# Performance work log

Hardware: AMD Instinct MI355X
Metric: run time of the kernel (lower is better)

Reference implementation:

```python
import jax, jax.numpy as jnp
import numpy as np

BS, IMG, P, GRID, NPATCH = 4, 224, 14, 16, 256
D, HID, NC, NDIST = 384, 2688, 1000, 7
BETA = 0.07
LN_EPS = 1e-6


def setup_inputs() -> dict:
    key = jax.random.key(0)
    ks = jax.random.split(key, 10)
    feat_target = jax.random.normal(ks[0], (BS, NPATCH, D), jnp.float32)
    feat_ref = jax.random.normal(ks[1], (BS, NPATCH, D), jnp.float32)
    labels_ref = jax.random.randint(ks[2], (BS, 1, IMG, IMG), 0, NC, jnp.int32)
    # distractor permutations of the batch (one per distractor sample)
    perms = jnp.argsort(jax.random.uniform(ks[3], (NDIST, BS)), axis=-1).astype(jnp.int32)
    # projector Mlp (fc1 -> GELU -> fc2), xavier-ish scaling
    fc1_w = jax.random.normal(ks[4], (D, HID), jnp.float32) * (1.0 / np.sqrt(D))
    fc1_b = jnp.zeros((HID,), jnp.float32)
    fc2_w = jax.random.normal(ks[5], (HID, D), jnp.float32) * (1.0 / np.sqrt(HID))
    fc2_b = jnp.zeros((D,), jnp.float32)
    ln_w = jnp.ones((D,), jnp.float32)
    ln_b = jnp.zeros((D,), jnp.float32)
    return {"feat_target": feat_target, "feat_ref": feat_ref, "labels_ref": labels_ref,
            "perms": perms, "fc1_w": fc1_w, "fc1_b": fc1_b, "fc2_w": fc2_w,
            "fc2_b": fc2_b, "ln_w": ln_w, "ln_b": ln_b}


def _layer_norm(x, w, b):
    mu = x.mean(-1, keepdims=True)
    var = jnp.mean((x - mu) ** 2, axis=-1, keepdims=True)
    return (x - mu) * jax.lax.rsqrt(var + LN_EPS) * w + b


def _l2norm(x, eps=1e-12):
    n = jnp.sqrt(jnp.sum(x * x, axis=-1, keepdims=True))
    return x / jnp.maximum(n, eps)


def reference(feat_target, feat_ref, labels_ref, perms, fc1_w, fc1_b, fc2_w, fc2_b, ln_w, ln_b):
    bs = feat_target.shape[0]

    def proj_norm(x):
        h = jax.nn.gelu(x @ fc1_w + fc1_b, approximate=False)  # torch nn.GELU (erf)
        return _layer_norm(h @ fc2_w + fc2_b, ln_w, ln_b)

    ft = proj_norm(feat_target)   # (bs, 256, 384)
    fr = proj_norm(feat_ref)      # (bs, 256, 384)

    # patchify ground truth: (bs,1,224,224) -> (bs, 256, 14*14)
    g = labels_ref.reshape(bs, 1, GRID, P, GRID, P).transpose(0, 2, 4, 1, 3, 5)
    g = g.reshape(bs, NPATCH, P * P)
    # per-patch class histogram / (P*P) == one_hot(...).mean(dim=3), without huge one-hot
    seg = (jnp.arange(NPATCH, dtype=jnp.int32)[None, :, None] * NC + g).reshape(bs, -1)
    counts = jax.vmap(lambda s: jax.ops.segment_sum(
        jnp.ones(s.shape, jnp.float32), s, num_segments=NPATCH * NC))(seg)
    label = counts.reshape(bs, NPATCH, NC) / float(P * P)  # (bs, 256, 1000)

    # distractors: block 0 is identity, blocks 1..NDIST are batch permutations
    all_perm = jnp.concatenate([jnp.arange(bs, dtype=perms.dtype)[None], perms], 0)  # (8, bs)
    lab_d = label[all_perm].transpose(1, 0, 2, 3).reshape(bs, -1, NC)   # (bs, 2048, 1000)
    feat_d = fr[all_perm].transpose(1, 0, 2, 3).reshape(bs, -1, D)      # (bs, 2048, 384)

    # cosine-similarity softmax cross attention (soft kNN over labels)
    q = _l2norm(ft)
    k = _l2norm(feat_d)
    attn = jax.nn.softmax(jnp.einsum('bqd,bkd->bqk', q, k) / BETA, axis=-1)
    label_hat = jnp.einsum('bqk,bkc->bqc', attn, lab_d)                 # (bs, 256, 1000)

    label_hat = label_hat.reshape(bs, GRID, GRID, NC).transpose(0, 3, 1, 2)
    # nearest upsample 16x16 -> 224x224 (scale 14 exactly)
    out = jnp.repeat(jnp.repeat(label_hat, P, axis=2), P, axis=3)
    return out
```

## Files before the change

### kernel.cpp

```cpp
#include <hip/hip_runtime.h>

#define BSZ 4
#define NPATCH 256
#define DIM 384
#define HID 2688
#define NCLS 1000
#define KTOT 2048
#define IMGSZ 224
#define PCH 14
#define GRD 16

static constexpr float INV_BETA = 1.0f / 0.07f;
static constexpr float LN_EPS_F = 1e-6f;

typedef unsigned short u16;
typedef unsigned int   u32;
typedef __attribute__((ext_vector_type(8))) __bf16 bf16x8;
typedef __attribute__((ext_vector_type(4))) float  f32x4;

#define WAITVM(n) asm volatile("s_waitcnt vmcnt(" #n ")" ::: "memory")

__device__ __forceinline__ u16 f2bf(float f) {
    u32 u = __float_as_uint(f);
    return (u16)((u + 0x7FFFu + ((u >> 16) & 1u)) >> 16);
}
__device__ __forceinline__ float bf2f(u16 h) {
    return __uint_as_float(((u32)h) << 16);
}
__device__ __forceinline__ f32x4 mfma16(bf16x8 a, bf16x8 b, f32x4 c) {
    return __builtin_amdgcn_mfma_f32_16x16x32_bf16(a, b, c, 0, 0, 0);
}
__device__ __forceinline__ void gll16(const u16* g, u16* l) {
    __builtin_amdgcn_global_load_lds(
        (const __attribute__((address_space(1))) void*)g,
        (__attribute__((address_space(3))) void*)l, 16, 0, 0);
}
__device__ __forceinline__ bf16x8 ld8(const u16* p) {
    return *(const bf16x8*)p;
}
__device__ __forceinline__ int swz(int row, int cseg) {
    return cseg ^ ((row >> 1) & 3);
}

__device__ __forceinline__ void transpose_split_body(
    const float* __restrict__ In, int R, int C, int bx, int by,
    u16* __restrict__ OutHi, u16* __restrict__ OutLo, float (*tile)[33])
{
    int cx = bx * 32, ry = by * 32;
    int t = threadIdx.x;
    int tr = t >> 5, tc = t & 31;
    #pragma unroll
    for (int i = 0; i < 4; ++i)
        tile[tr + i * 8][tc] = In[(size_t)(ry + tr + i * 8) * C + cx + tc];
    __syncthreads();
    int a = t >> 3, seg = t & 7;
    u16 h4[4], l4[4];
    #pragma unroll
    for (int i = 0; i < 4; ++i) {
        float v = tile[seg * 4 + i][a];
        h4[i] = f2bf(v);
        l4[i] = f2bf(v - bf2f(h4[i]));
    }
    size_t off = (size_t)(cx + a) * R + ry + seg * 4;
    *(uint2*)(OutHi + off) = make_uint2((u32)h4[0] | ((u32)h4[1] << 16),
                                        (u32)h4[2] | ((u32)h4[3] << 16));
    *(uint2*)(OutLo + off) = make_uint2((u32)l4[0] | ((u32)l4[1] << 16),
                                        (u32)l4[2] | ((u32)l4[3] << 16));
}

__global__ __launch_bounds__(256) void prep_kernel(
    const float* __restrict__ Xt, const float* __restrict__ Xr,
    const float* __restrict__ fc1w, const float* __restrict__ fc2w,
    const int* __restrict__ labels,
    u16* __restrict__ Xhi, u16* __restrict__ Xlo,
    u16* __restrict__ W1Th, u16* __restrict__ W1Tl,
    u16* __restrict__ W2Th, u16* __restrict__ W2Tl,
    u16* __restrict__ LabT)
{
    __shared__ float tile[32][33];
    __shared__ int hist16[16][NCLS];
    int blk = blockIdx.x, t = threadIdx.x;
    if (blk < 768) {
        int e = (blk * 256 + t) * 4;
        const float* src = (e < 1024 * DIM) ? (Xt + e) : (Xr + e - 1024 * DIM);
        float4 v = *(const float4*)src;
        float x[4] = {v.x, v.y, v.z, v.w};
        u16 h[4], l[4];
        #pragma unroll
        for (int i = 0; i < 4; ++i) {
            h[i] = f2bf(x[i]);
            l[i] = f2bf(x[i] - bf2f(h[i]));
        }
        *(uint2*)(Xhi + e) = make_uint2((u32)h[0] | ((u32)h[1] << 16), (u32)h[2] | ((u32)h[3] << 16));
        *(uint2*)(Xlo + e) = make_uint2((u32)l[0] | ((u32)l[1] << 16), (u32)l[2] | ((u32)l[3] << 16));
    } else if (blk < 1776) {
        int i = blk - 768;
        transpose_split_body(fc1w, DIM, HID, i % (HID / 32), i / (HID / 32), W1Th, W1Tl, tile);
    } else if (blk < 2784) {
        int i = blk - 1776;
        transpose_split_body(fc2w, HID, DIM, i % (DIM / 32), i / (DIM / 32), W2Th, W2Tl, tile);
    } else {
        int bp = blk - 2784;
        int b = bp >> 4, py = bp & 15;
        for (int u = t; u < 16 * NCLS; u += 256) ((int*)hist16)[u] = 0;
        __syncthreads();
        const int* lrow = labels + (size_t)b * IMGSZ * IMGSZ + py * PCH * IMGSZ;
        for (int i = t; i < PCH * IMGSZ; i += 256) {
            int lab = lrow[i];
            int px = (i % IMGSZ) / PCH;
            atomicAdd(&hist16[px][lab], 1);
        }
        __syncthreads();
        const float inv = 1.0f / (PCH * PCH);
        for (int u = t; u < 16 * NCLS; u += 256) {
            int c = u >> 4, px = u & 15;
            LabT[((size_t)(b << 10) + c) * 256 + py * 16 + px] =
                f2bf(hist16[px][c] * inv);
        }
    }
}

template<int MODE>
__global__ __launch_bounds__(256) void gemm64(
    const u16* __restrict__ Ahi, const u16* __restrict__ Alo,
    const u16* __restrict__ Bhi, const u16* __restrict__ Blo,
    const float* __restrict__ bias,
    u16* __restrict__ OutHi, u16* __restrict__ OutLo, float* __restrict__ OutF)
{
    constexpr int K  = (MODE == 1) ? HID : DIM;
    constexpr int KS = (MODE == 1) ? HID / 4 : K;
    constexpr int NT = KS / 32;
    constexpr int N  = (MODE == 0) ? HID : DIM;

    __shared__ u16 As_h[3][128 * 32];
    __shared__ u16 As_l[3][128 * 32];
    __shared__ u16 Bs_h[3][64 * 32];
    __shared__ u16 Bs_l[3][64 * 32];

    const int tid = threadIdx.x, lane = tid & 63, wid = tid >> 6;
    const int wm = wid >> 1, wn = wid & 1;
    int n0, m0;
    if constexpr (MODE == 0) {
        int s = (blockIdx.x & 7) * 84 + (blockIdx.x >> 3);
        n0 = (s % 42) * 64;
        m0 = (s / 42) * 128;
    } else {
        n0 = blockIdx.x * 64;
        m0 = blockIdx.y * 128;
    }

    const u16 *a_h, *a_l, *b_h, *b_l;
    if constexpr (MODE == 0) {
        a_h = Ahi + (size_t)m0 * K;   a_l = Alo + (size_t)m0 * K;
        b_h = Bhi + (size_t)n0 * K;   b_l = Blo + (size_t)n0 * K;
    } else {
        const int kbase = blockIdx.z * KS;
        a_h = Ahi + (size_t)m0 * K + kbase;   a_l = Alo + (size_t)m0 * K + kbase;
        b_h = Bhi + (size_t)n0 * K + kbase;   b_l = Blo + (size_t)n0 * K + kbase;
    }

    auto stage = [&](int buf, int k0) {
        #pragma unroll
        for (int j = 0; j < 2; ++j) {
            int g = j * 256 + tid;
            int row = g >> 2, cs = g & 3;
            int col = swz(row, cs) << 3;
            gll16(a_h + (size_t)row * K + k0 + col, &As_h[buf][g * 8]);
            gll16(a_l + (size_t)row * K + k0 + col, &As_l[buf][g * 8]);
        }
        {
            int row = tid >> 2, cs = tid & 3;
            int col = swz(row, cs) << 3;
            gll16(b_h + (size_t)row * K + k0 + col, &Bs_h[buf][tid * 8]);
            gll16(b_l + (size_t)row * K + k0 + col, &Bs_l[buf][tid * 8]);
        }
    };

    const int l15 = lane & 15, cq = lane >> 4;
    int aoff[4], boff[2];
    #pragma unroll
    for (int i = 0; i < 4; ++i) {
        int ra = wm * 64 + i * 16 + l15;
        aoff[i] = ra * 32 + swz(ra, cq) * 8;
    }
    #pragma unroll
    for (int j = 0; j < 2; ++j) {
        int rb = wn * 32 + j * 16 + l15;
        boff[j] = rb * 32 + swz(rb, cq) * 8;
    }

    f32x4 acc[4][2] = {};

    auto compute = [&](int buf) {
        bf16x8 ah[4], al[4], bh[2], bl[2];
        #pragma unroll
        for (int i = 0; i < 4; ++i) {
            ah[i] = ld8(&As_h[buf][aoff[i]]);
            al[i] = ld8(&As_l[buf][aoff[i]]);
        }
        #pragma unroll
        for (int j = 0; j < 2; ++j) {
            bh[j] = ld8(&Bs_h[buf][boff[j]]);
            bl[j] = ld8(&Bs_l[buf][boff[j]]);
        }
        #pragma unroll
        for (int mi = 0; mi < 4; ++mi)
            #pragma unroll
            for (int ni = 0; ni < 2; ++ni) {
                acc[mi][ni] = mfma16(ah[mi], bh[ni], acc[mi][ni]);
                acc[mi][ni] = mfma16(ah[mi], bl[ni], acc[mi][ni]);
                acc[mi][ni] = mfma16(al[mi], bh[ni], acc[mi][ni]);
            }
    };

    stage(0, 0);
    stage(1, 32);
    int cur = 0;
    for (int t = 0; t < NT - 1; ++t) {
        WAITVM(6);
        __builtin_amdgcn_s_barrier();
        __builtin_amdgcn_sched_barrier(0);
        if (t + 2 < NT) {
            int nb = cur + 2; if (nb >= 3) nb -= 3;
            stage(nb, (t + 2) * 32);
        }
        compute(cur);
        cur = (cur == 2) ? 0 : cur + 1;
    }
    WAITVM(0);
    __builtin_amdgcn_s_barrier();
    __builtin_amdgcn_sched_barrier(0);
    compute(cur);

    #pragma unroll
    for (int mi = 0; mi < 4; ++mi)
        #pragma unroll
        for (int ni = 0; ni < 2; ++ni)
            #pragma unroll
            for (int r = 0; r < 4; ++r) {
                int gm = m0 + wm * 64 + mi * 16 + cq * 4 + r;
                int gn = n0 + wn * 32 + ni * 16 + l15;
                float v = acc[mi][ni][r];
                if constexpr (MODE == 0) {
                    v += bias[gn];
                    v = 0.5f * v * (1.0f + erff(v * 0.7071067811865476f));
                    u16 h = f2bf(v);
                    OutHi[(size_t)gm * N + gn] = h;
                    OutLo[(size_t)gm * N + gn] = f2bf(v - bf2f(h));
                } else {
                    OutF[(size_t)blockIdx.z * (2048 * DIM) + (size_t)gm * N + gn] = v;
                }
            }
}

__global__ __launch_bounds__(256) void qk64(
    const u16* __restrict__ Z, const int* __restrict__ perms,
    u16* __restrict__ E, float* __restrict__ R)
{
    constexpr int NT = DIM / 32;
    __shared__ u16 As[3][64 * 32];
    __shared__ u16 Bs[3][64 * 32];

    const int tid = threadIdx.x, lane = tid & 63, wid = tid >> 6;
    const int wm = wid >> 1, wn = wid & 1;
    const int n0 = blockIdx.x * 64, m0 = blockIdx.y * 64, b = blockIdx.z;
    const int d = n0 >> 8;
    const int apd = (d == 0) ? b : perms[(d - 1) * BSZ + b];

    const u16* a_g = Z + (size_t)(b * NPATCH + m0) * DIM;
    const u16* b_g = Z + (size_t)(1024 + apd * NPATCH + (n0 & 255)) * DIM;

    auto stage = [&](int buf, int k0) {
        int row = tid >> 2, cs = tid & 3;
        int col = swz(row, cs) << 3;
        gll16(a_g + (size_t)row * DIM + k0 + col, &As[buf][tid * 8]);
        gll16(b_g + (size_t)row * DIM + k0 + col, &Bs[buf][tid * 8]);
    };

    const int l15 = lane & 15, cq = lane >> 4;
    int aoff[2], boff[2];
    #pragma unroll
    for (int i = 0; i < 2; ++i) {
        int ra = wm * 32 + i * 16 + l15;
        aoff[i] = ra * 32 + swz(ra, cq) * 8;
        int rb = wn * 32 + i * 16 + l15;
        boff[i] = rb * 32 + swz(rb, cq) * 8;
    }

    f32x4 acc[2][2] = {};
    auto compute = [&](int buf) {
        bf16x8 a[2], bb[2];
        #pragma unroll
        for (int i = 0; i < 2; ++i) {
            a[i] = ld8(&As[buf][aoff[i]]);
            bb[i] = ld8(&Bs[buf][boff[i]]);
        }
        #pragma unroll
        for (int mi = 0; mi < 2; ++mi)
            #pragma unroll
            for (int ni = 0; ni < 2; ++ni)
                acc[mi][ni] = mfma16(a[mi], bb[ni], acc[mi][ni]);
    };

    stage(0, 0);
    stage(1, 32);
    int cur = 0;
    for (int t = 0; t < NT - 1; ++t) {
        WAITVM(2);
        __builtin_amdgcn_s_barrier();
        __builtin_amdgcn_sched_barrier(0);
        if (t + 2 < NT) {
            int nb = cur + 2; if (nb >= 3) nb -= 3;
            stage(nb, (t + 2) * 32);
        }
        compute(cur);
        cur = (cur == 2) ? 0 : cur + 1;
    }
    WAITVM(0);
    __builtin_amdgcn_s_barrier();
    __builtin_amdgcn_sched_barrier(0);
    compute(cur);

    float rp[2][4] = {};
    #pragma unroll
    for (int mi = 0; mi < 2; ++mi)
        #pragma unroll
        for (int ni = 0; ni < 2; ++ni)
            #pragma unroll
            for (int r = 0; r < 4; ++r) {
                int gm = m0 + wm * 32 + mi * 16 + cq * 4 + r;
                int gn = n0 + wn * 32 + ni * 16 + l15;
                float e = expf((acc[mi][ni][r] - 1.0f) * INV_BETA);
                u16 h = f2bf(e);
                E[((size_t)b * NPATCH + gm) * KTOT + gn] = h;
                rp[mi][r] += bf2f(h);
            }
    #pragma unroll
    for (int mi = 0; mi < 2; ++mi)
        #pragma unroll
        for (int r = 0; r < 4; ++r) {
            float v = rp[mi][r];
            #pragma unroll
            for (int off = 1; off < 16; off <<= 1) v += __shfl_xor(v, off);
            if (l15 == 0) {
                int gm = m0 + wm * 32 + mi * 16 + cq * 4 + r;
                atomicAdd(&R[(size_t)b * NPATCH + gm], v);
            }
        }
}

__global__ __launch_bounds__(256) void pv64(
    const u16* __restrict__ E, const u16* __restrict__ LabT,
    const int* __restrict__ perms, float* __restrict__ Lp)
{
    constexpr int KSP = KTOT / 4;
    constexpr int NT  = KSP / 32;
    __shared__ u16 As[3][128 * 32];
    __shared__ u16 Bs[3][64 * 32];

    const int tid = threadIdx.x, lane = tid & 63, wid = tid >> 6;
    const int wm = wid >> 1, wn = wid & 1;
    const int n0 = blockIdx.x * 64, m0 = blockIdx.y * 128;
    const int b = blockIdx.z & 3, ks = blockIdx.z >> 2;
    const int s0 = ks * 2;
    const int apd0 = (s0 == 0) ? b : perms[(s0 - 1) * BSZ + b];
    const int apd1 = perms[s0 * BSZ + b];

    const u16* abase = E + (size_t)(b * NPATCH + m0) * KTOT + ks * KSP;

    auto stage = [&](int buf, int k0) {
        #pragma unroll
        for (int j = 0; j < 2; ++j) {
            int g = j * 256 + tid;
            int row = g >> 2, cs = g & 3;
            int col = swz(row, cs) << 3;
            gll16(abase + (size_t)row * KTOT + k0 + col, &As[buf][g * 8]);
        }
        {
            int apd = (k0 & 256) ? apd1 : apd0;
            int p0 = k0 & 255;
            int row = tid >> 2, cs = tid & 3;
            int col = swz(row, cs) << 3;
            gll16(LabT + ((size_t)(apd << 10) + n0 + row) * 256 + p0 + col,
                  &Bs[buf][tid * 8]);
        }
    };

    const int l15 = lane & 15, cq = lane >> 4;
    int aoff[4], boff[2];
    #pragma unroll
    for (int i = 0; i < 4; ++i) {
        int ra = wm * 64 + i * 16 + l15;
        aoff[i] = ra * 32 + swz(ra, cq) * 8;
    }
    #pragma unroll
    for (int j = 0; j < 2; ++j) {
        int rb = wn * 32 + j * 16 + l15;
        boff[j] = rb * 32 + swz(rb, cq) * 8;
    }

    f32x4 acc[4][2] = {};
    auto compute = [&](int buf) {
        bf16x8 a[4], bb[2];
        #pragma unroll
        for (int i = 0; i < 4; ++i) a[i] = ld8(&As[buf][aoff[i]]);
        #pragma unroll
        for (int j = 0; j < 2; ++j) bb[j] = ld8(&Bs[buf][boff[j]]);
        #pragma unroll
        for (int mi = 0; mi < 4; ++mi)
            #pragma unroll
            for (int ni = 0; ni < 2; ++ni)
                acc[mi][ni] = mfma16(a[mi], bb[ni], acc[mi][ni]);
    };

    stage(0, 0);
    stage(1, 32);
    int cur = 0;
    for (int t = 0; t < NT - 1; ++t) {
        WAITVM(3);
        __builtin_amdgcn_s_barrier();
        __builtin_amdgcn_sched_barrier(0);
        if (t + 2 < NT) {
            int nb = cur + 2; if (nb >= 3) nb -= 3;
            stage(nb, (t + 2) * 32);
        }
        compute(cur);
        cur = (cur == 2) ? 0 : cur + 1;
    }
    WAITVM(0);
    __builtin_amdgcn_s_barrier();
    __builtin_amdgcn_sched_barrier(0);
    compute(cur);

    #pragma unroll
    for (int mi = 0; mi < 4; ++mi)
        #pragma unroll
        for (int ni = 0; ni < 2; ++ni) {
            int gn = n0 + wn * 32 + ni * 16 + l15;
            if (gn < NCLS) {
                #pragma unroll
                for (int r = 0; r < 4; ++r) {
                    int gm = m0 + wm * 64 + mi * 16 + cq * 4 + r;
                    Lp[(((size_t)ks * BSZ + b) * NPATCH + gm) * NCLS + gn] =
                        acc[mi][ni][r];
                }
            }
        }
}

__device__ __forceinline__ float wave_sum(float v) {
    #pragma unroll
    for (int off = 32; off > 0; off >>= 1) v += __shfl_xor(v, off);
    return v;
}

__global__ __launch_bounds__(256) void ln_l2_kernel(
    const float* __restrict__ P0, const float* __restrict__ fc2b,
    const float* __restrict__ w, const float* __restrict__ b,
    u16* __restrict__ Zbf)
{
    const float* P1 = P0 + 1 * 2048 * DIM;
    const float* P2 = P0 + 2 * 2048 * DIM;
    const float* P3 = P0 + 3 * 2048 * DIM;
    int wid = threadIdx.x >> 6, lane = threadIdx.x & 63;
    int row = blockIdx.x * 4 + wid;
    size_t base = (size_t)row * DIM;
    float x[6];
    float s = 0.0f;
    #pragma unroll
    for (int i = 0; i < 6; ++i) {
        int c = lane + 64 * i;
        x[i] = ((P0[base + c] + P1[base + c]) + (P2[base + c] + P3[base + c])) + fc2b[c];
        s += x[i];
    }
    s = wave_sum(s);
    float mu = s * (1.0f / DIM);
    float vs = 0.0f;
    #pragma unroll
    for (int i = 0; i < 6; ++i) { float d = x[i] - mu; vs += d * d; }
    vs = wave_sum(vs);
    float rstd = 1.0f / sqrtf(vs * (1.0f / DIM) + LN_EPS_F);
    float z[6];
    float n2 = 0.0f;
    #pragma unroll
    for (int i = 0; i < 6; ++i) {
        z[i] = (x[i] - mu) * rstd * w[lane + 64 * i] + b[lane + 64 * i];
        n2 += z[i] * z[i];
    }
    n2 = wave_sum(n2);
    float inv = 1.0f / fmaxf(sqrtf(n2), 1e-12f);
    #pragma unroll
    for (int i = 0; i < 6; ++i)
        Zbf[base + lane + 64 * i] = f2bf(z[i] * inv);
}

__global__ __launch_bounds__(256) void upsample_kernel(
    const float* __restrict__ Lp, const float* __restrict__ R,
    float* __restrict__ out)
{
    constexpr size_t S = (size_t)BSZ * NPATCH * NCLS;
    int blk = blockIdx.x;
    int gy = blk & 15;
    int bc = blk >> 4;
    int c = bc % NCLS;
    int b = bc / NCLS;
    __shared__ float vals[GRD];
    int t = threadIdx.x;
    if (t < GRD) {
        int q = b * NPATCH + gy * GRD + t;
        size_t i = (size_t)q * NCLS + c;
        vals[t] = ((Lp[i] + Lp[i + S]) + (Lp[i + 2 * S] + Lp[i + 3 * S])) / R[q];
    }
    __syncthreads();
    float* obase = out + ((size_t)(b * NCLS + c) * IMGSZ + gy * PCH) * IMGSZ;
    for (int idx = t; idx < PCH * 56; idx += 256) {
        int x4 = idx % 56, dy = idx / 56;
        int x0 = x4 * 4;
        f32x4 v = {vals[x0 / PCH], vals[(x0 + 1) / PCH],
                   vals[(x0 + 2) / PCH], vals[(x0 + 3) / PCH]};
        __builtin_nontemporal_store(v, (f32x4*)(obase + dy * IMGSZ + x0));
    }
}

extern "C" void kernel_launch(void* const* d_in, const int* in_sizes, int n_in,
                              void* d_out, int out_size, void* d_ws, size_t ws_size,
                              hipStream_t stream)
{
    (void)in_sizes; (void)n_in; (void)out_size; (void)ws_size;
    const float* feat_t = (const float*)d_in[0];
    const float* feat_r = (const float*)d_in[1];
    const int*   labels = (const int*)d_in[2];
    const int*   perms  = (const int*)d_in[3];
    const float* fc1_w  = (const float*)d_in[4];
    const float* fc1_b  = (const float*)d_in[5];
    const float* fc2_w  = (const float*)d_in[6];
    const float* fc2_b  = (const float*)d_in[7];
    const float* ln_w   = (const float*)d_in[8];
    const float* ln_b   = (const float*)d_in[9];
    float* out = (float*)d_out;
    char*  W   = (char*)d_ws;

    u16*   Hhi  = (u16*)(W + 0);
    u16*   Hlo  = (u16*)(W + 11010048);
    u16*   E    = (u16*)(W + 0);
    float* R    = (float*)(W + 4194304);
    float* Lp   = (float*)(W + 4718592);
    float* P0   = (float*)(W + 22020096);
    u16*   Zbf  = (u16*)(W + 34603008);
    u16*   LabT = (u16*)(W + 37748736);
    u16*   Xhi  = (u16*)(W + 39845888);
    u16*   Xlo  = (u16*)(W + 41418752);
    u16*   W1Th = (u16*)(W + 42991616);
    u16*   W1Tl = (u16*)(W + 45056000);
    u16*   W2Th = (u16*)(W + 47120384);
    u16*   W2Tl = (u16*)(W + 49184768);

    prep_kernel<<<dim3(2848), dim3(256), 0, stream>>>(
        feat_t, feat_r, fc1_w, fc2_w, labels,
        Xhi, Xlo, W1Th, W1Tl, W2Th, W2Tl, LabT);

    gemm64<0><<<dim3(672), dim3(256), 0, stream>>>(
        Xhi, Xlo, W1Th, W1Tl, fc1_b, Hhi, Hlo, nullptr);

    gemm64<1><<<dim3(6, 16, 4), dim3(256), 0, stream>>>(
        Hhi, Hlo, W2Th, W2Tl, nullptr, nullptr, nullptr, P0);

    ln_l2_kernel<<<dim3(2048 / 4), dim3(256), 0, stream>>>(P0, fc2_b, ln_w, ln_b, Zbf);

    hipMemsetAsync(R, 0, BSZ * NPATCH * sizeof(float), stream);

    qk64<<<dim3(32, 4, 4), dim3(256), 0, stream>>>(Zbf, perms, E, R);

    pv64<<<dim3(16, 2, 16), dim3(256), 0, stream>>>(E, LabT, perms, Lp);

    upsample_kernel<<<dim3(BSZ * NCLS * GRD), dim3(256), 0, stream>>>(Lp, R, out);
}
```

Before: 264.2 us.

## Drop split-bf16 emulation in projector GEMMs; fold R memset into LayerNorm kernel

The projector GEMMs previously emulated fp32 accuracy with split hi/lo bf16 operands and three MFMAs per tile. They now use plain single bf16 operands with one MFMA per tile, which cuts the operand traffic, LDS footprint and MFMA count roughly threefold. The separate memset of the row-sum buffer is also folded into the LayerNorm kernel, removing one launch. The risk is lower precision in the projector outputs, which feed a softmax with temperature 0.07 that amplifies small errors and could push results past tolerance.

```diff
diff --git a/kernel.cpp b/kernel.cpp
--- a/kernel.cpp
+++ b/kernel.cpp
@@ -42,9 +42,9 @@
     return cseg ^ ((row >> 1) & 3);
 }
 
-__device__ __forceinline__ void transpose_split_body(
+__device__ __forceinline__ void transpose_cast_body(
     const float* __restrict__ In, int R, int C, int bx, int by,
-    u16* __restrict__ OutHi, u16* __restrict__ OutLo, float (*tile)[33])
+    u16* __restrict__ OutT, float (*tile)[33])
 {
     int cx = bx * 32, ry = by * 32;
     int t = threadIdx.x;
@@ -54,27 +54,20 @@
         tile[tr + i * 8][tc] = In[(size_t)(ry + tr + i * 8) * C + cx + tc];
     __syncthreads();
     int a = t >> 3, seg = t & 7;
-    u16 h4[4], l4[4];
-    #pragma unroll
-    for (int i = 0; i < 4; ++i) {
-        float v = tile[seg * 4 + i][a];
-        h4[i] = f2bf(v);
-        l4[i] = f2bf(v - bf2f(h4[i]));
-    }
+    u16 h4[4];
+    #pragma unroll
+    for (int i = 0; i < 4; ++i)
+        h4[i] = f2bf(tile[seg * 4 + i][a]);
     size_t off = (size_t)(cx + a) * R + ry + seg * 4;
-    *(uint2*)(OutHi + off) = make_uint2((u32)h4[0] | ((u32)h4[1] << 16),
-                                        (u32)h4[2] | ((u32)h4[3] << 16));
-    *(uint2*)(OutLo + off) = make_uint2((u32)l4[0] | ((u32)l4[1] << 16),
-                                        (u32)l4[2] | ((u32)l4[3] << 16));
+    *(uint2*)(OutT + off) = make_uint2((u32)h4[0] | ((u32)h4[1] << 16),
+                                       (u32)h4[2] | ((u32)h4[3] << 16));
 }
 
 __global__ __launch_bounds__(256) void prep_kernel(
     const float* __restrict__ Xt, const float* __restrict__ Xr,
     const float* __restrict__ fc1w, const float* __restrict__ fc2w,
     const int* __restrict__ labels,
-    u16* __restrict__ Xhi, u16* __restrict__ Xlo,
-    u16* __restrict__ W1Th, u16* __restrict__ W1Tl,
-    u16* __restrict__ W2Th, u16* __restrict__ W2Tl,
+    u16* __restrict__ Xbf, u16* __restrict__ W1T, u16* __restrict__ W2T,
     u16* __restrict__ LabT)
 {
     __shared__ float tile[32][33];
@@ -84,21 +77,15 @@
         int e = (blk * 256 + t) * 4;
         const float* src = (e < 1024 * DIM) ? (Xt + e) : (Xr + e - 1024 * DIM);
         float4 v = *(const float4*)src;
-        float x[4] = {v.x, v.y, v.z, v.w};
-        u16 h[4], l[4];
-        #pragma unroll
-        for (int i = 0; i < 4; ++i) {
-            h[i] = f2bf(x[i]);
-            l[i] = f2bf(x[i] - bf2f(h[i]));
-        }
-        *(uint2*)(Xhi + e) = make_uint2((u32)h[0] | ((u32)h[1] << 16), (u32)h[2] | ((u32)h[3] << 16));
-        *(uint2*)(Xlo + e) = make_uint2((u32)l[0] | ((u32)l[1] << 16), (u32)l[2] | ((u32)l[3] << 16));
+        u16 h[4] = {f2bf(v.x), f2bf(v.y), f2bf(v.z), f2bf(v.w)};
+        *(uint2*)(Xbf + e) = make_uint2((u32)h[0] | ((u32)h[1] << 16),
+                                        (u32)h[2] | ((u32)h[3] << 16));
     } else if (blk < 1776) {
         int i = blk - 768;
-        transpose_split_body(fc1w, DIM, HID, i % (HID / 32), i / (HID / 32), W1Th, W1Tl, tile);
+        transpose_cast_body(fc1w, DIM, HID, i % (HID / 32), i / (HID / 32), W1T, tile);
     } else if (blk < 2784) {
         int i = blk - 1776;
-        transpose_split_body(fc2w, HID, DIM, i % (DIM / 32), i / (DIM / 32), W2Th, W2Tl, tile);
+        transpose_cast_body(fc2w, HID, DIM, i % (DIM / 32), i / (DIM / 32), W2T, tile);
     } else {
         int bp = blk - 2784;
         int b = bp >> 4, py = bp & 15;
@@ -122,20 +109,17 @@
 
 template<int MODE>
 __global__ __launch_bounds__(256) void gemm64(
-    const u16* __restrict__ Ahi, const u16* __restrict__ Alo,
-    const u16* __restrict__ Bhi, const u16* __restrict__ Blo,
+    const u16* __restrict__ A_g, const u16* __restrict__ B_g,
     const float* __restrict__ bias,
-    u16* __restrict__ OutHi, u16* __restrict__ OutLo, float* __restrict__ OutF)
+    u16* __restrict__ OutB, float* __restrict__ OutF)
 {
     constexpr int K  = (MODE == 1) ? HID : DIM;
     constexpr int KS = (MODE == 1) ? HID / 4 : K;
     constexpr int NT = KS / 32;
     constexpr int N  = (MODE == 0) ? HID : DIM;
 
-    __shared__ u16 As_h[3][128 * 32];
-    __shared__ u16 As_l[3][128 * 32];
-    __shared__ u16 Bs_h[3][64 * 32];
-    __shared__ u16 Bs_l[3][64 * 32];
+    __shared__ u16 As[3][128 * 32];
+    __shared__ u16 Bs[3][64 * 32];
 
     const int tid = threadIdx.x, lane = tid & 63, wid = tid >> 6;
     const int wm = wid >> 1, wn = wid & 1;
@@ -149,15 +133,9 @@
         m0 = blockIdx.y * 128;
     }
 
-    const u16 *a_h, *a_l, *b_h, *b_l;
-    if constexpr (MODE == 0) {
-        a_h = Ahi + (size_t)m0 * K;   a_l = Alo + (size_t)m0 * K;
-        b_h = Bhi + (size_t)n0 * K;   b_l = Blo + (size_t)n0 * K;
-    } else {
-        const int kbase = blockIdx.z * KS;
-        a_h = Ahi + (size_t)m0 * K + kbase;   a_l = Alo + (size_t)m0 * K + kbase;
-        b_h = Bhi + (size_t)n0 * K + kbase;   b_l = Blo + (size_t)n0 * K + kbase;
-    }
+    const int kbase = (MODE == 1) ? blockIdx.z * KS : 0;
+    const u16* a_g = A_g + (size_t)m0 * K + kbase;
+    const u16* b_g = B_g + (size_t)n0 * K + kbase;
 
     auto stage = [&](int buf, int k0) {
         #pragma unroll
@@ -165,14 +143,12 @@
             int g = j * 256 + tid;
             int row = g >> 2, cs = g & 3;
             int col = swz(row, cs) << 3;
-            gll16(a_h + (size_t)row * K + k0 + col, &As_h[buf][g * 8]);
-            gll16(a_l + (size_t)row * K + k0 + col, &As_l[buf][g * 8]);
+            gll16(a_g + (size_t)row * K + k0 + col, &As[buf][g * 8]);
         }
         {
             int row = tid >> 2, cs = tid & 3;
             int col = swz(row, cs) << 3;
-            gll16(b_h + (size_t)row * K + k0 + col, &Bs_h[buf][tid * 8]);
-            gll16(b_l + (size_t)row * K + k0 + col, &Bs_l[buf][tid * 8]);
+            gll16(b_g + (size_t)row * K + k0 + col, &Bs[buf][tid * 8]);
         }
     };
 
@@ -192,32 +168,23 @@
     f32x4 acc[4][2] = {};
 
     auto compute = [&](int buf) {
-        bf16x8 ah[4], al[4], bh[2], bl[2];
-        #pragma unroll
-        for (int i = 0; i < 4; ++i) {
-            ah[i] = ld8(&As_h[buf][aoff[i]]);
-            al[i] = ld8(&As_l[buf][aoff[i]]);
-        }
-        #pragma unroll
-        for (int j = 0; j < 2; ++j) {
-            bh[j] = ld8(&Bs_h[buf][boff[j]]);
-            bl[j] = ld8(&Bs_l[buf][boff[j]]);
-        }
+        bf16x8 a[4], bb[2];
+        #pragma unroll
+        for (int i = 0; i < 4; ++i) a[i] = ld8(&As[buf][aoff[i]]);
+        #pragma unroll
+        for (int j = 0; j < 2; ++j) bb[j] = ld8(&Bs[buf][boff[j]]);
         #pragma unroll
         for (int mi = 0; mi < 4; ++mi)
             #pragma unroll
-            for (int ni = 0; ni < 2; ++ni) {
-                acc[mi][ni] = mfma16(ah[mi], bh[ni], acc[mi][ni]);
-                acc[mi][ni] = mfma16(ah[mi], bl[ni], acc[mi][ni]);
-                acc[mi][ni] = mfma16(al[mi], bh[ni], acc[mi][ni]);
-            }
+            for (int ni = 0; ni < 2; ++ni)
+                acc[mi][ni] = mfma16(a[mi], bb[ni], acc[mi][ni]);
     };
 
     stage(0, 0);
     stage(1, 32);
     int cur = 0;
     for (int t = 0; t < NT - 1; ++t) {
-        WAITVM(6);
+        WAITVM(3);
         __builtin_amdgcn_s_barrier();
         __builtin_amdgcn_sched_barrier(0);
         if (t + 2 < NT) {
@@ -244,9 +211,7 @@
                 if constexpr (MODE == 0) {
                     v += bias[gn];
                     v = 0.5f * v * (1.0f + erff(v * 0.7071067811865476f));
-                    u16 h = f2bf(v);
-                    OutHi[(size_t)gm * N + gn] = h;
-                    OutLo[(size_t)gm * N + gn] = f2bf(v - bf2f(h));
+                    OutB[(size_t)gm * N + gn] = f2bf(v);
                 } else {
                     OutF[(size_t)blockIdx.z * (2048 * DIM) + (size_t)gm * N + gn] = v;
                 }
@@ -457,8 +422,10 @@
 __global__ __launch_bounds__(256) void ln_l2_kernel(
     const float* __restrict__ P0, const float* __restrict__ fc2b,
     const float* __restrict__ w, const float* __restrict__ b,
-    u16* __restrict__ Zbf)
-{
+    u16* __restrict__ Zbf, float* __restrict__ R)
+{
+    if (blockIdx.x < 256 && threadIdx.x < 4)
+        R[blockIdx.x * 4 + threadIdx.x] = 0.0f;
     const float* P1 = P0 + 1 * 2048 * DIM;
     const float* P2 = P0 + 2 * 2048 * DIM;
     const float* P3 = P0 + 3 * 2048 * DIM;
@@ -540,34 +507,28 @@
     float* out = (float*)d_out;
     char*  W   = (char*)d_ws;
 
-    u16*   Hhi  = (u16*)(W + 0);
-    u16*   Hlo  = (u16*)(W + 11010048);
+    u16*   H    = (u16*)(W + 0);
     u16*   E    = (u16*)(W + 0);
     float* R    = (float*)(W + 4194304);
     float* Lp   = (float*)(W + 4718592);
     float* P0   = (float*)(W + 22020096);
     u16*   Zbf  = (u16*)(W + 34603008);
     u16*   LabT = (u16*)(W + 37748736);
-    u16*   Xhi  = (u16*)(W + 39845888);
-    u16*   Xlo  = (u16*)(W + 41418752);
-    u16*   W1Th = (u16*)(W + 42991616);
-    u16*   W1Tl = (u16*)(W + 45056000);
-    u16*   W2Th = (u16*)(W + 47120384);
-    u16*   W2Tl = (u16*)(W + 49184768);
+    u16*   Xbf  = (u16*)(W + 39845888);
+    u16*   W1T  = (u16*)(W + 42991616);
+    u16*   W2T  = (u16*)(W + 47120384);
 
     prep_kernel<<<dim3(2848), dim3(256), 0, stream>>>(
-        feat_t, feat_r, fc1_w, fc2_w, labels,
-        Xhi, Xlo, W1Th, W1Tl, W2Th, W2Tl, LabT);
+        feat_t, feat_r, fc1_w, fc2_w, labels, Xbf, W1T, W2T, LabT);
 
     gemm64<0><<<dim3(672), dim3(256), 0, stream>>>(
-        Xhi, Xlo, W1Th, W1Tl, fc1_b, Hhi, Hlo, nullptr);
+        Xbf, W1T, fc1_b, H, nullptr);
 
     gemm64<1><<<dim3(6, 16, 4), dim3(256), 0, stream>>>(
-        Hhi, Hlo, W2Th, W2Tl, nullptr, nullptr, nullptr, P0);
-
-    ln_l2_kernel<<<dim3(2048 / 4), dim3(256), 0, stream>>>(P0, fc2_b, ln_w, ln_b, Zbf);
-
-    hipMemsetAsync(R, 0, BSZ * NPATCH * sizeof(float), stream);
+        H, W2T, nullptr, nullptr, P0);
+
+    ln_l2_kernel<<<dim3(2048 / 4), dim3(256), 0, stream>>>(
+        P0, fc2_b, ln_w, ln_b, Zbf, R);
 
     qk64<<<dim3(32, 4, 4), dim3(256), 0, stream>>>(Zbf, perms, E, R);
 
```

Measured after the change: 226.1 us. -14.4%, faster.
